# Optimization experiments

Hardware: AMD Instinct MI355X
Metric: run time of the kernel (lower is better)

The kernel has to match this reference:

```python
import jax, jax.numpy as jnp
import numpy as np

NEG_SLOPE = 0.2
EPS = 1e-16


def add_self_loops(edge_index, num_nodes):
    loops = jnp.arange(num_nodes, dtype=edge_index.dtype)
    loops = jnp.stack([loops, loops])  # [2, N]
    return jnp.concatenate([edge_index, loops], axis=1)


def gat_conv(x, edge_index, W, att_src, att_dst, bias, heads, out_c, concat):
    # x: [N, F_in]; edge_index: [2, E] (src row 0 -> dst row 1)
    N = x.shape[0]
    h = (x @ W).reshape(N, heads, out_c)            # [N, H, C]
    src, dst = edge_index[0], edge_index[1]
    a_src = (h * att_src).sum(-1)                    # [N, H]
    a_dst = (h * att_dst).sum(-1)                    # [N, H]
    e = a_src[src] + a_dst[dst]                      # [E, H]
    e = jnp.where(e > 0, e, NEG_SLOPE * e)           # leaky_relu
    # segment softmax over destination node
    m = jax.ops.segment_max(e, dst, num_segments=N)  # [N, H]
    ex = jnp.exp(e - m[dst])                         # [E, H]
    denom = jax.ops.segment_sum(ex, dst, num_segments=N)  # [N, H]
    alpha = ex / (denom[dst] + EPS)                  # [E, H]
    msg = alpha[:, :, None] * h[src]                 # [E, H, C]
    out = jax.ops.segment_sum(msg, dst, num_segments=N)   # [N, H, C]
    if concat:
        out = out.reshape(N, heads * out_c)
    else:
        out = out.mean(axis=1)
    return out + bias


def setup_inputs() -> dict:
    key = jax.random.key(0)
    ks = jax.random.split(key, 12)
    N, E, F_IN, HID, H1, OUT = 100000, 1600000, 512, 8, 8, 40
    x = jax.random.normal(ks[0], (N, F_IN), dtype=jnp.float32)
    edge_index = jax.random.randint(ks[1], (2, E), 0, N, dtype=jnp.int64)
    glorot = lambda k, shp: jax.random.normal(k, shp, jnp.float32) * jnp.sqrt(2.0 / (shp[0] + shp[-1]))
    W1 = glorot(ks[2], (F_IN, H1 * HID))
    att_src1 = glorot(ks[3], (H1, HID))
    att_dst1 = glorot(ks[4], (H1, HID))
    b1 = jnp.zeros((H1 * HID,), jnp.float32)
    W2 = glorot(ks[5], (H1 * HID, 1 * OUT))
    att_src2 = glorot(ks[6], (1, OUT))
    att_dst2 = glorot(ks[7], (1, OUT))
    b2 = jnp.zeros((OUT,), jnp.float32)
    return {"x": x, "edge_index": edge_index, "W1": W1, "att_src1": att_src1,
            "att_dst1": att_dst1, "b1": b1, "W2": W2, "att_src2": att_src2,
            "att_dst2": att_dst2, "b2": b2}


def reference(x, edge_index, W1, att_src1, att_dst1, b1, W2, att_src2, att_dst2, b2):
    N = x.shape[0]
    ei = add_self_loops(edge_index, N)
    h = gat_conv(x, ei, W1, att_src1, att_dst1, b1, heads=8, out_c=8, concat=True)
    h = jax.nn.relu(h)
    # dropout p=0.0 / eval mode -> identity
    out = gat_conv(h, ei, W2, att_src2, att_dst2, b2, heads=1, out_c=40, concat=False)
    return jax.nn.log_softmax(out, axis=1)
```

## Files before the change

### kernel.cpp

```cpp
#include <hip/hip_runtime.h>
#include <math.h>

#define NEG_SLOPE 0.2f
#define EPS_DEN 1e-16f

__device__ __forceinline__ float leaky(float v) { return v > 0.f ? v : NEG_SLOPE * v; }

typedef __attribute__((ext_vector_type(8))) short bf16x8;
typedef __attribute__((ext_vector_type(4))) float f32x4;

__device__ __forceinline__ unsigned bf16rne(float f) {
    unsigned u = __float_as_uint(f);
    return (u + 0x7FFFu + ((u >> 16) & 1u)) >> 16;
}
__device__ __forceinline__ unsigned pack2(float a, float b) {
    unsigned r;
    asm("v_cvt_pk_bf16_f32 %0, %1, %2" : "=v"(r) : "v"(a), "v"(b));
    return r;
}
__device__ __forceinline__ float bfu(unsigned short u) {
    return __uint_as_float(((unsigned)u) << 16);
}

__global__ __launch_bounds__(256) void gemm1_mfma(
    const float* __restrict__ x, const float* __restrict__ W1,
    unsigned short* __restrict__ h1b, int N)
{
    __shared__ __align__(16) unsigned short As[128 * 40];
    __shared__ __align__(16) unsigned short Bs[64 * 40];

    const int t = threadIdx.x;
    const int w = t >> 6;
    const int lane = t & 63;
    const int m16 = lane & 15;
    const int quad = lane >> 4;
    const int rowBase = blockIdx.x * 128;

    f32x4 acc[2][4];
#pragma unroll
    for (int i = 0; i < 2; ++i)
#pragma unroll
        for (int j = 0; j < 4; ++j) acc[i][j] = (f32x4){0.f, 0.f, 0.f, 0.f};

    const float4* x4 = (const float4*)x;

#pragma unroll 1
    for (int chunk = 0; chunk < 16; ++chunk) {
        const int k0 = chunk * 32;
#pragma unroll
        for (int r = 0; r < 4; ++r) {
            int e = t + r * 256;
            int row = e >> 3;
            int kg = e & 7;
            int grow = rowBase + row;
            float4 v = make_float4(0.f, 0.f, 0.f, 0.f);
            if (grow < N) v = x4[(size_t)grow * 128 + (k0 >> 2) + kg];
            uint2 pk = make_uint2(pack2(v.x, v.y), pack2(v.z, v.w));
            *(uint2*)&As[row * 40 + kg * 4] = pk;
        }
        {
            int c = lane;
            int jb = w * 8;
            float f[8];
#pragma unroll
            for (int j = 0; j < 8; ++j) f[j] = W1[(size_t)(k0 + jb + j) * 64 + c];
            uint4 pk;
            pk.x = pack2(f[0], f[1]); pk.y = pack2(f[2], f[3]);
            pk.z = pack2(f[4], f[5]); pk.w = pack2(f[6], f[7]);
            *(uint4*)&Bs[c * 40 + jb] = pk;
        }
        __syncthreads();
        bf16x8 a0 = *(const bf16x8*)&As[(w * 32 + m16) * 40 + quad * 8];
        bf16x8 a1 = *(const bf16x8*)&As[(w * 32 + 16 + m16) * 40 + quad * 8];
#pragma unroll
        for (int j = 0; j < 4; ++j) {
            bf16x8 b = *(const bf16x8*)&Bs[(j * 16 + m16) * 40 + quad * 8];
            acc[0][j] = __builtin_amdgcn_mfma_f32_16x16x32_bf16(a0, b, acc[0][j], 0, 0, 0);
            acc[1][j] = __builtin_amdgcn_mfma_f32_16x16x32_bf16(a1, b, acc[1][j], 0, 0, 0);
        }
        __syncthreads();
    }

#pragma unroll
    for (int i = 0; i < 2; ++i)
#pragma unroll
        for (int reg = 0; reg < 4; ++reg) {
            int r = rowBase + w * 32 + i * 16 + quad * 4 + reg;
            if (r < N) {
#pragma unroll
                for (int j = 0; j < 4; ++j)
                    h1b[(size_t)r * 64 + j * 16 + m16] = (unsigned short)bf16rne(acc[i][j][reg]);
            }
        }
}

__global__ __launch_bounds__(256) void att1_kernel(
    const unsigned short* __restrict__ h1b, const float* __restrict__ att_src,
    const float* __restrict__ att_dst, float* __restrict__ a_src,
    float* __restrict__ a_dst, int N)
{
    int g = blockIdx.x * 256 + threadIdx.x;
    int row = g >> 3, h = g & 7;
    if (row >= N) return;
    uint4 pk = *(const uint4*)(h1b + (size_t)row * 64 + h * 8);
    float v[8];
    v[0] = __uint_as_float(pk.x << 16); v[1] = __uint_as_float(pk.x & 0xFFFF0000u);
    v[2] = __uint_as_float(pk.y << 16); v[3] = __uint_as_float(pk.y & 0xFFFF0000u);
    v[4] = __uint_as_float(pk.z << 16); v[5] = __uint_as_float(pk.z & 0xFFFF0000u);
    v[6] = __uint_as_float(pk.w << 16); v[7] = __uint_as_float(pk.w & 0xFFFF0000u);
    float ps = 0.f, pd = 0.f;
#pragma unroll
    for (int c = 0; c < 8; ++c) {
        ps += v[c] * att_src[h * 8 + c];
        pd += v[c] * att_dst[h * 8 + c];
    }
    a_src[(size_t)row * 8 + h] = ps;
    a_dst[(size_t)row * 8 + h] = pd;
}

__global__ __launch_bounds__(256) void deg_kernel(
    const int* __restrict__ ei, unsigned* __restrict__ deg, int E, int Etot)
{
    int idx = blockIdx.x * blockDim.x + threadIdx.x;
    if (idx >= Etot) return;
    int d = (idx < E) ? ei[E + idx] : (idx - E);
    atomicAdd(&deg[d], 1u);
}

__global__ __launch_bounds__(256) void scanA_kernel(
    const unsigned* __restrict__ deg, unsigned* __restrict__ loc,
    unsigned* __restrict__ bsum, int N)
{
    __shared__ unsigned sh[256];
    int i = blockIdx.x * 256 + threadIdx.x;
    unsigned v = (i < N) ? deg[i] : 0u;
    sh[threadIdx.x] = v;
    __syncthreads();
    for (int off = 1; off < 256; off <<= 1) {
        unsigned u = (threadIdx.x >= (unsigned)off) ? sh[threadIdx.x - off] : 0u;
        __syncthreads();
        sh[threadIdx.x] += u;
        __syncthreads();
    }
    if (i < N) loc[i] = sh[threadIdx.x] - v;
    if (threadIdx.x == 255) bsum[blockIdx.x] = sh[255];
}

__global__ __launch_bounds__(1024) void scanB_kernel(unsigned* __restrict__ bsum, int nb)
{
    __shared__ unsigned sh[1024];
    int t = threadIdx.x;
    unsigned carry = 0;
    for (int base = 0; base < nb; base += 1024) {
        int i = base + t;
        unsigned v = (i < nb) ? bsum[i] : 0u;
        sh[t] = v;
        __syncthreads();
        for (int off = 1; off < 1024; off <<= 1) {
            unsigned u = (t >= off) ? sh[t - off] : 0u;
            __syncthreads();
            sh[t] += u;
            __syncthreads();
        }
        unsigned incl = sh[t];
        unsigned tot  = sh[1023];
        __syncthreads();
        if (i < nb) bsum[i] = incl - v + carry;
        carry += tot;
        __syncthreads();
    }
}

__global__ __launch_bounds__(256) void scanC_kernel(
    const unsigned* __restrict__ loc, const unsigned* __restrict__ bsum,
    unsigned* __restrict__ rowstart, unsigned* __restrict__ cursor, int N, int Etot)
{
    int i = blockIdx.x * 256 + threadIdx.x;
    if (i >= N) return;
    unsigned r = loc[i] + bsum[blockIdx.x];
    rowstart[i] = r;
    cursor[i] = r;
    if (i == 0) rowstart[N] = (unsigned)Etot;
}

__global__ __launch_bounds__(256) void scatter_kernel(
    const int* __restrict__ ei, unsigned* __restrict__ cursor,
    int* __restrict__ csr_src, int E, int Etot, int sliceW)
{
    int slice = blockIdx.x & 7;
    int idx = (blockIdx.x >> 3) * 256 + threadIdx.x;
    if (idx >= Etot) return;
    int d = (idx < E) ? ei[E + idx] : (idx - E);
    int lo = slice * sliceW;
    if (d < lo || d >= lo + sliceW) return;
    int s = (idx < E) ? ei[idx] : d;
    unsigned pos = atomicAdd(&cursor[d], 1u);
    csr_src[pos] = s;
}

__global__ __launch_bounds__(256) void aggr1_kernel(
    const unsigned* __restrict__ rowstart, const int* __restrict__ csr_src,
    const float* __restrict__ a_src, const float* __restrict__ a_dst,
    const unsigned short* __restrict__ h1b, const float* __restrict__ b1,
    float* __restrict__ h2, int N)
{
    int g = blockIdx.x * 4 + (threadIdx.x >> 6);
    int lane = threadIdx.x & 63;
    if (g >= N) return;
    int h = lane >> 3;
    float ad = a_dst[(size_t)g * 8 + h];
    unsigned k0 = rowstart[g], k1 = rowstart[g + 1];
    float acc0 = 0.f, acc1 = 0.f, acc2 = 0.f, acc3 = 0.f;
    float dn0 = 0.f, dn1 = 0.f, dn2 = 0.f, dn3 = 0.f;
    unsigned k = k0;
    for (; k + 4 <= k1; k += 4) {
        int s0 = csr_src[k],     s1 = csr_src[k + 1];
        int s2 = csr_src[k + 2], s3 = csr_src[k + 3];
        float p0 = __expf(leaky(a_src[(size_t)s0 * 8 + h] + ad));
        float p1 = __expf(leaky(a_src[(size_t)s1 * 8 + h] + ad));
        float p2 = __expf(leaky(a_src[(size_t)s2 * 8 + h] + ad));
        float p3 = __expf(leaky(a_src[(size_t)s3 * 8 + h] + ad));
        acc0 += p0 * bfu(h1b[(size_t)s0 * 64 + lane]); dn0 += p0;
        acc1 += p1 * bfu(h1b[(size_t)s1 * 64 + lane]); dn1 += p1;
        acc2 += p2 * bfu(h1b[(size_t)s2 * 64 + lane]); dn2 += p2;
        acc3 += p3 * bfu(h1b[(size_t)s3 * 64 + lane]); dn3 += p3;
    }
    for (; k < k1; ++k) {
        int s0 = csr_src[k];
        float p0 = __expf(leaky(a_src[(size_t)s0 * 8 + h] + ad));
        acc0 += p0 * bfu(h1b[(size_t)s0 * 64 + lane]); dn0 += p0;
    }
    float den = (dn0 + dn1) + (dn2 + dn3);
    float acc = (acc0 + acc1) + (acc2 + acc3);
    float v = acc / (den + EPS_DEN) + b1[lane];
    h2[(size_t)g * 64 + lane] = v > 0.f ? v : 0.f;
}

__global__ __launch_bounds__(256) void gemm2_kernel(
    const float* __restrict__ h2, const float* __restrict__ W2,
    const float* __restrict__ att_src2, const float* __restrict__ att_dst2,
    unsigned short* __restrict__ h3b32, unsigned short* __restrict__ h3b8,
    float* __restrict__ a_src, float* __restrict__ a_dst, int N)
{
    __shared__ float Wl[64 * 40];
    int t = threadIdx.x;
    for (int i = t; i < 64 * 40; i += 256) Wl[i] = W2[i];
    __syncthreads();
    int lane = t & 63, wy = t >> 6;
    int row = blockIdx.x * 4 + wy;
    if (row >= N) return;
    float acc = 0.f;
    const float* hr = h2 + (size_t)row * 64;
    if (lane < 40) {
#pragma unroll 8
        for (int k = 0; k < 64; ++k) acc += hr[k] * Wl[k * 40 + lane];
        if (lane < 32) h3b32[(size_t)row * 32 + lane] = (unsigned short)bf16rne(acc);
        else           h3b8[(size_t)row * 8 + (lane - 32)] = (unsigned short)bf16rne(acc);
    }
    float ps = (lane < 40) ? acc * att_src2[lane] : 0.f;
    float pd = (lane < 40) ? acc * att_dst2[lane] : 0.f;
#pragma unroll
    for (int off = 32; off; off >>= 1) { ps += __shfl_down(ps, off); pd += __shfl_down(pd, off); }
    if (lane == 0) { a_src[row] = ps; a_dst[row] = pd; }
}

__global__ __launch_bounds__(256) void aggr2_kernel(
    const unsigned* __restrict__ rowstart, const int* __restrict__ csr_src,
    const float* __restrict__ a_src, const float* __restrict__ a_dst,
    const unsigned short* __restrict__ h3b32, const unsigned short* __restrict__ h3b8,
    const float* __restrict__ b2, float* __restrict__ y, int N)
{
    int g = blockIdx.x * 4 + (threadIdx.x >> 6);
    int lane = threadIdx.x & 63;
    if (g >= N) return;
    const bool valid = lane < 40;
    const unsigned short* hsrc = (lane < 32) ? h3b32 : h3b8;
    const int rowmul = (lane < 32) ? 32 : 8;
    const int cidx   = (lane < 32) ? lane : (valid ? lane - 32 : 0);
    float ad = a_dst[g];
    unsigned k0 = rowstart[g], k1 = rowstart[g + 1];
    float acc0 = 0.f, acc1 = 0.f, acc2 = 0.f, acc3 = 0.f;
    float dn0 = 0.f, dn1 = 0.f, dn2 = 0.f, dn3 = 0.f;
    unsigned k = k0;
    for (; k + 4 <= k1; k += 4) {
        int s0 = csr_src[k],     s1 = csr_src[k + 1];
        int s2 = csr_src[k + 2], s3 = csr_src[k + 3];
        float p0 = __expf(leaky(a_src[s0] + ad));
        float p1 = __expf(leaky(a_src[s1] + ad));
        float p2 = __expf(leaky(a_src[s2] + ad));
        float p3 = __expf(leaky(a_src[s3] + ad));
        float hv0 = bfu(hsrc[(size_t)s0 * rowmul + cidx]);
        float hv1 = bfu(hsrc[(size_t)s1 * rowmul + cidx]);
        float hv2 = bfu(hsrc[(size_t)s2 * rowmul + cidx]);
        float hv3 = bfu(hsrc[(size_t)s3 * rowmul + cidx]);
        if (!valid) { hv0 = hv1 = hv2 = hv3 = 0.f; }
        acc0 += p0 * hv0; dn0 += p0;
        acc1 += p1 * hv1; dn1 += p1;
        acc2 += p2 * hv2; dn2 += p2;
        acc3 += p3 * hv3; dn3 += p3;
    }
    for (; k < k1; ++k) {
        int s0 = csr_src[k];
        float p0 = __expf(leaky(a_src[s0] + ad));
        float hv0 = valid ? bfu(hsrc[(size_t)s0 * rowmul + cidx]) : 0.f;
        acc0 += p0 * hv0; dn0 += p0;
    }
    float den = (dn0 + dn1) + (dn2 + dn3);
    float acc = (acc0 + acc1) + (acc2 + acc3);
    float v = valid ? (acc / (den + EPS_DEN) + b2[lane]) : -INFINITY;
    float mx = v;
#pragma unroll
    for (int off = 32; off; off >>= 1) mx = fmaxf(mx, __shfl_down(mx, off));
    mx = __shfl(mx, 0);
    float ex = valid ? expf(v - mx) : 0.f;
    float ss = ex;
#pragma unroll
    for (int off = 32; off; off >>= 1) ss += __shfl_down(ss, off);
    ss = __shfl(ss, 0);
    if (valid) y[(size_t)g * 40 + lane] = v - mx - logf(ss);
}

extern "C" void kernel_launch(void* const* d_in, const int* in_sizes, int n_in,
                              void* d_out, int out_size, void* d_ws, size_t ws_size,
                              hipStream_t stream)
{
    const float* x        = (const float*)d_in[0];
    const int*   ei       = (const int*)d_in[1];
    const float* W1       = (const float*)d_in[2];
    const float* att_src1 = (const float*)d_in[3];
    const float* att_dst1 = (const float*)d_in[4];
    const float* b1       = (const float*)d_in[5];
    const float* W2       = (const float*)d_in[6];
    const float* att_src2 = (const float*)d_in[7];
    const float* att_dst2 = (const float*)d_in[8];
    const float* b2       = (const float*)d_in[9];
    float* y = (float*)d_out;

    int N = in_sizes[0] / 512;
    int E = in_sizes[1] / 2;
    int Etot = E + N;
    int nb = (N + 255) / 256;
    int sliceW = (N + 7) / 8;

    char* p = (char*)d_ws;
    unsigned short* h1b = (unsigned short*)p; p += (size_t)N * 64 * 2;
    float* a_src1a  = (float*)p;   p += (size_t)N * 8 * 4;
    float* a_dst1a  = (float*)p;   p += (size_t)N * 8 * 4;
    float* h2       = (float*)p;   p += (size_t)N * 64 * 4;
    unsigned short* h3b32 = (unsigned short*)p; p += (size_t)N * 32 * 2;
    unsigned short* h3b8  = (unsigned short*)p; p += (size_t)N * 8 * 2;
    float* a_src2a  = (float*)p;   p += (size_t)N * 4;
    float* a_dst2a  = (float*)p;   p += (size_t)N * 4;
    unsigned* deg   = (unsigned*)p; p += (size_t)N * 4;
    unsigned* loc   = (unsigned*)p; p += (size_t)N * 4;
    unsigned* bsum  = (unsigned*)p; p += (size_t)nb * 4;
    unsigned* rowstart = (unsigned*)p; p += (size_t)(N + 1) * 4;
    unsigned* cursor   = (unsigned*)p; p += (size_t)N * 4;
    int* csr_src    = (int*)p;     p += (size_t)Etot * 4;

    hipMemsetAsync(deg, 0, (size_t)N * 4, stream);

    gemm1_mfma<<<(N + 127) / 128, 256, 0, stream>>>(x, W1, h1b, N);
    att1_kernel<<<(N * 8 + 255) / 256, 256, 0, stream>>>(h1b, att_src1, att_dst1, a_src1a, a_dst1a, N);

    deg_kernel<<<(Etot + 255) / 256, 256, 0, stream>>>(ei, deg, E, Etot);
    scanA_kernel<<<nb, 256, 0, stream>>>(deg, loc, bsum, N);
    scanB_kernel<<<1, 1024, 0, stream>>>(bsum, nb);
    scanC_kernel<<<nb, 256, 0, stream>>>(loc, bsum, rowstart, cursor, N, Etot);
    scatter_kernel<<<8 * ((Etot + 255) / 256), 256, 0, stream>>>(ei, cursor, csr_src, E, Etot, sliceW);

    aggr1_kernel<<<(N + 3) / 4, 256, 0, stream>>>(rowstart, csr_src, a_src1a, a_dst1a, h1b, b1, h2, N);

    gemm2_kernel<<<(N + 3) / 4, 256, 0, stream>>>(h2, W2, att_src2, att_dst2, h3b32, h3b8, a_src2a, a_dst2a, N);

    aggr2_kernel<<<(N + 3) / 4, 256, 0, stream>>>(rowstart, csr_src, a_src2a, a_dst2a, h3b32, h3b8, b2, y, N);
}
```

Baseline: 692.4 us.

## Fuse attention logits into GEMM1 epilogue and split wavefront across edges in aggregation

Computes the layer-1 attention dot products inside the MFMA GEMM epilogue using cross-lane shuffles, which removes the separate att1 kernel and its re-read of h1. Both aggregation kernels now have each half-wave take alternate edges and load packed pairs of bf16 values. Partial sums are combined with a shuffle at the end, so more edges are in flight per wave while each lane issues fewer loads. The attention logits are now computed from fp32 accumulators rather than bf16-rounded values, and the epilogue picks up extra shuffle work.

```diff
diff --git a/kernel.cpp b/kernel.cpp
--- a/kernel.cpp
+++ b/kernel.cpp
@@ -24,7 +24,9 @@
 
 __global__ __launch_bounds__(256) void gemm1_mfma(
     const float* __restrict__ x, const float* __restrict__ W1,
-    unsigned short* __restrict__ h1b, int N)
+    const float* __restrict__ att_src1, const float* __restrict__ att_dst1,
+    unsigned short* __restrict__ h1b, float* __restrict__ a_src,
+    float* __restrict__ a_dst, int N)
 {
     __shared__ __align__(16) unsigned short As[128 * 40];
     __shared__ __align__(16) unsigned short Bs[64 * 40];
@@ -81,6 +83,13 @@
         __syncthreads();
     }
 
+    float ats[4], atd[4];
+#pragma unroll
+    for (int j = 0; j < 4; ++j) {
+        ats[j] = att_src1[j * 16 + m16];
+        atd[j] = att_dst1[j * 16 + m16];
+    }
+
 #pragma unroll
     for (int i = 0; i < 2; ++i)
 #pragma unroll
@@ -88,34 +97,22 @@
             int r = rowBase + w * 32 + i * 16 + quad * 4 + reg;
             if (r < N) {
 #pragma unroll
-                for (int j = 0; j < 4; ++j)
-                    h1b[(size_t)r * 64 + j * 16 + m16] = (unsigned short)bf16rne(acc[i][j][reg]);
+                for (int j = 0; j < 4; ++j) {
+                    float val = acc[i][j][reg];
+                    h1b[(size_t)r * 64 + j * 16 + m16] = (unsigned short)bf16rne(val);
+                    float ps = val * ats[j];
+                    float pd = val * atd[j];
+                    ps += __shfl_xor(ps, 1); pd += __shfl_xor(pd, 1);
+                    ps += __shfl_xor(ps, 2); pd += __shfl_xor(pd, 2);
+                    ps += __shfl_xor(ps, 4); pd += __shfl_xor(pd, 4);
+                    if ((m16 & 7) == 0) {
+                        int head = j * 2 + (m16 >> 3);
+                        a_src[(size_t)r * 8 + head] = ps;
+                        a_dst[(size_t)r * 8 + head] = pd;
+                    }
+                }
             }
         }
-}
-
-__global__ __launch_bounds__(256) void att1_kernel(
-    const unsigned short* __restrict__ h1b, const float* __restrict__ att_src,
-    const float* __restrict__ att_dst, float* __restrict__ a_src,
-    float* __restrict__ a_dst, int N)
-{
-    int g = blockIdx.x * 256 + threadIdx.x;
-    int row = g >> 3, h = g & 7;
-    if (row >= N) return;
-    uint4 pk = *(const uint4*)(h1b + (size_t)row * 64 + h * 8);
-    float v[8];
-    v[0] = __uint_as_float(pk.x << 16); v[1] = __uint_as_float(pk.x & 0xFFFF0000u);
-    v[2] = __uint_as_float(pk.y << 16); v[3] = __uint_as_float(pk.y & 0xFFFF0000u);
-    v[4] = __uint_as_float(pk.z << 16); v[5] = __uint_as_float(pk.z & 0xFFFF0000u);
-    v[6] = __uint_as_float(pk.w << 16); v[7] = __uint_as_float(pk.w & 0xFFFF0000u);
-    float ps = 0.f, pd = 0.f;
-#pragma unroll
-    for (int c = 0; c < 8; ++c) {
-        ps += v[c] * att_src[h * 8 + c];
-        pd += v[c] * att_dst[h * 8 + c];
-    }
-    a_src[(size_t)row * 8 + h] = ps;
-    a_dst[(size_t)row * 8 + h] = pd;
 }
 
 __global__ __launch_bounds__(256) void deg_kernel(
@@ -207,33 +204,47 @@
     int g = blockIdx.x * 4 + (threadIdx.x >> 6);
     int lane = threadIdx.x & 63;
     if (g >= N) return;
-    int h = lane >> 3;
+    int half = lane >> 5;
+    int l = lane & 31;
+    int h = l >> 2;
     float ad = a_dst[(size_t)g * 8 + h];
+    const unsigned* h1u = (const unsigned*)h1b;
     unsigned k0 = rowstart[g], k1 = rowstart[g + 1];
-    float acc0 = 0.f, acc1 = 0.f, acc2 = 0.f, acc3 = 0.f;
-    float dn0 = 0.f, dn1 = 0.f, dn2 = 0.f, dn3 = 0.f;
+    float ax0 = 0.f, ay0 = 0.f, ax1 = 0.f, ay1 = 0.f;
+    float dn0 = 0.f, dn1 = 0.f;
     unsigned k = k0;
     for (; k + 4 <= k1; k += 4) {
-        int s0 = csr_src[k],     s1 = csr_src[k + 1];
-        int s2 = csr_src[k + 2], s3 = csr_src[k + 3];
+        int e0 = k + half, e1 = k + 2 + half;
+        int s0 = csr_src[e0], s1 = csr_src[e1];
         float p0 = __expf(leaky(a_src[(size_t)s0 * 8 + h] + ad));
         float p1 = __expf(leaky(a_src[(size_t)s1 * 8 + h] + ad));
-        float p2 = __expf(leaky(a_src[(size_t)s2 * 8 + h] + ad));
-        float p3 = __expf(leaky(a_src[(size_t)s3 * 8 + h] + ad));
-        acc0 += p0 * bfu(h1b[(size_t)s0 * 64 + lane]); dn0 += p0;
-        acc1 += p1 * bfu(h1b[(size_t)s1 * 64 + lane]); dn1 += p1;
-        acc2 += p2 * bfu(h1b[(size_t)s2 * 64 + lane]); dn2 += p2;
-        acc3 += p3 * bfu(h1b[(size_t)s3 * 64 + lane]); dn3 += p3;
-    }
-    for (; k < k1; ++k) {
-        int s0 = csr_src[k];
-        float p0 = __expf(leaky(a_src[(size_t)s0 * 8 + h] + ad));
-        acc0 += p0 * bfu(h1b[(size_t)s0 * 64 + lane]); dn0 += p0;
-    }
-    float den = (dn0 + dn1) + (dn2 + dn3);
-    float acc = (acc0 + acc1) + (acc2 + acc3);
-    float v = acc / (den + EPS_DEN) + b1[lane];
-    h2[(size_t)g * 64 + lane] = v > 0.f ? v : 0.f;
+        unsigned v0 = h1u[(size_t)s0 * 32 + l];
+        unsigned v1 = h1u[(size_t)s1 * 32 + l];
+        ax0 += p0 * bfu((unsigned short)v0); ay0 += p0 * bfu((unsigned short)(v0 >> 16)); dn0 += p0;
+        ax1 += p1 * bfu((unsigned short)v1); ay1 += p1 * bfu((unsigned short)(v1 >> 16)); dn1 += p1;
+    }
+    for (; k < k1; k += 2) {
+        unsigned e = k + half;
+        if (e < k1) {
+            int s = csr_src[e];
+            float p = __expf(leaky(a_src[(size_t)s * 8 + h] + ad));
+            unsigned v = h1u[(size_t)s * 32 + l];
+            ax0 += p * bfu((unsigned short)v); ay0 += p * bfu((unsigned short)(v >> 16)); dn0 += p;
+        }
+    }
+    float ax = ax0 + ax1, ay = ay0 + ay1, dn = dn0 + dn1;
+    ax += __shfl_xor(ax, 32);
+    ay += __shfl_xor(ay, 32);
+    dn += __shfl_xor(dn, 32);
+    if (half == 0) {
+        float inv = 1.f / (dn + EPS_DEN);
+        float vx = ax * inv + b1[2 * l];
+        float vy = ay * inv + b1[2 * l + 1];
+        float2 o;
+        o.x = vx > 0.f ? vx : 0.f;
+        o.y = vy > 0.f ? vy : 0.f;
+        *(float2*)&h2[(size_t)g * 64 + 2 * l] = o;
+    }
 }
 
 __global__ __launch_bounds__(256) void gemm2_kernel(
@@ -273,51 +284,57 @@
     int g = blockIdx.x * 4 + (threadIdx.x >> 6);
     int lane = threadIdx.x & 63;
     if (g >= N) return;
-    const bool valid = lane < 40;
-    const unsigned short* hsrc = (lane < 32) ? h3b32 : h3b8;
-    const int rowmul = (lane < 32) ? 32 : 8;
-    const int cidx   = (lane < 32) ? lane : (valid ? lane - 32 : 0);
+    int half = lane >> 5;
+    int l = lane & 31;
+    const bool valid = l < 20;
+    const unsigned* hsrc = (l < 16) ? (const unsigned*)h3b32 : (const unsigned*)h3b8;
+    const int rowmul = (l < 16) ? 16 : 4;
+    const int cidx   = (l < 16) ? l : (valid ? l - 16 : 0);
     float ad = a_dst[g];
     unsigned k0 = rowstart[g], k1 = rowstart[g + 1];
-    float acc0 = 0.f, acc1 = 0.f, acc2 = 0.f, acc3 = 0.f;
-    float dn0 = 0.f, dn1 = 0.f, dn2 = 0.f, dn3 = 0.f;
+    float ax0 = 0.f, ay0 = 0.f, ax1 = 0.f, ay1 = 0.f;
+    float dn0 = 0.f, dn1 = 0.f;
     unsigned k = k0;
     for (; k + 4 <= k1; k += 4) {
-        int s0 = csr_src[k],     s1 = csr_src[k + 1];
-        int s2 = csr_src[k + 2], s3 = csr_src[k + 3];
+        int e0 = k + half, e1 = k + 2 + half;
+        int s0 = csr_src[e0], s1 = csr_src[e1];
         float p0 = __expf(leaky(a_src[s0] + ad));
         float p1 = __expf(leaky(a_src[s1] + ad));
-        float p2 = __expf(leaky(a_src[s2] + ad));
-        float p3 = __expf(leaky(a_src[s3] + ad));
-        float hv0 = bfu(hsrc[(size_t)s0 * rowmul + cidx]);
-        float hv1 = bfu(hsrc[(size_t)s1 * rowmul + cidx]);
-        float hv2 = bfu(hsrc[(size_t)s2 * rowmul + cidx]);
-        float hv3 = bfu(hsrc[(size_t)s3 * rowmul + cidx]);
-        if (!valid) { hv0 = hv1 = hv2 = hv3 = 0.f; }
-        acc0 += p0 * hv0; dn0 += p0;
-        acc1 += p1 * hv1; dn1 += p1;
-        acc2 += p2 * hv2; dn2 += p2;
-        acc3 += p3 * hv3; dn3 += p3;
-    }
-    for (; k < k1; ++k) {
-        int s0 = csr_src[k];
-        float p0 = __expf(leaky(a_src[s0] + ad));
-        float hv0 = valid ? bfu(hsrc[(size_t)s0 * rowmul + cidx]) : 0.f;
-        acc0 += p0 * hv0; dn0 += p0;
-    }
-    float den = (dn0 + dn1) + (dn2 + dn3);
-    float acc = (acc0 + acc1) + (acc2 + acc3);
-    float v = valid ? (acc / (den + EPS_DEN) + b2[lane]) : -INFINITY;
-    float mx = v;
-#pragma unroll
-    for (int off = 32; off; off >>= 1) mx = fmaxf(mx, __shfl_down(mx, off));
-    mx = __shfl(mx, 0);
-    float ex = valid ? expf(v - mx) : 0.f;
+        unsigned v0 = valid ? hsrc[(size_t)s0 * rowmul + cidx] : 0u;
+        unsigned v1 = valid ? hsrc[(size_t)s1 * rowmul + cidx] : 0u;
+        ax0 += p0 * bfu((unsigned short)v0); ay0 += p0 * bfu((unsigned short)(v0 >> 16)); dn0 += p0;
+        ax1 += p1 * bfu((unsigned short)v1); ay1 += p1 * bfu((unsigned short)(v1 >> 16)); dn1 += p1;
+    }
+    for (; k < k1; k += 2) {
+        unsigned e = k + half;
+        if (e < k1) {
+            int s = csr_src[e];
+            float p = __expf(leaky(a_src[s] + ad));
+            unsigned v = valid ? hsrc[(size_t)s * rowmul + cidx] : 0u;
+            ax0 += p * bfu((unsigned short)v); ay0 += p * bfu((unsigned short)(v >> 16)); dn0 += p;
+        }
+    }
+    float ax = ax0 + ax1, ay = ay0 + ay1, dn = dn0 + dn1;
+    ax += __shfl_xor(ax, 32);
+    ay += __shfl_xor(ay, 32);
+    dn += __shfl_xor(dn, 32);
+    float inv = 1.f / (dn + EPS_DEN);
+    float vx = valid ? (ax * inv + b2[2 * l]) : -INFINITY;
+    float vy = valid ? (ay * inv + b2[2 * l + 1]) : -INFINITY;
+    float mx = fmaxf(vx, vy);
+#pragma unroll
+    for (int off = 16; off; off >>= 1) mx = fmaxf(mx, __shfl_xor(mx, off));
+    float ex = valid ? (__expf(vx - mx) + __expf(vy - mx)) : 0.f;
     float ss = ex;
 #pragma unroll
-    for (int off = 32; off; off >>= 1) ss += __shfl_down(ss, off);
-    ss = __shfl(ss, 0);
-    if (valid) y[(size_t)g * 40 + lane] = v - mx - logf(ss);
+    for (int off = 16; off; off >>= 1) ss += __shfl_xor(ss, off);
+    float lse = mx + __logf(ss);
+    if (half == 0 && valid) {
+        float2 o;
+        o.x = vx - lse;
+        o.y = vy - lse;
+        *(float2*)&y[(size_t)g * 40 + 2 * l] = o;
+    }
 }
 
 extern "C" void kernel_launch(void* const* d_in, const int* in_sizes, int n_in,
@@ -360,8 +377,7 @@
 
     hipMemsetAsync(deg, 0, (size_t)N * 4, stream);
 
-    gemm1_mfma<<<(N + 127) / 128, 256, 0, stream>>>(x, W1, h1b, N);
-    att1_kernel<<<(N * 8 + 255) / 256, 256, 0, stream>>>(h1b, att_src1, att_dst1, a_src1a, a_dst1a, N);
+    gemm1_mfma<<<(N + 127) / 128, 256, 0, stream>>>(x, W1, att_src1, att_dst1, h1b, a_src1a, a_dst1a, N);
 
     deg_kernel<<<(Etot + 255) / 256, 256, 0, stream>>>(ei, deg, E, Etot);
     scanA_kernel<<<nb, 256, 0, stream>>>(deg, loc, bsum, N);
```

After: 679.1 us. No clear change (-1.9%).
